# Kernel optimization log

Hardware: AMD Instinct MI355X
Metric: run time of the kernel (lower is better)

The kernel has to match this reference:

```python
import jax, jax.numpy as jnp
import numpy as np

B, S, H, M = 32, 512, 1024, 8  # batch, seq_len, HP_hidden_dim, term_span (max span length)


def setup_inputs() -> dict:
    key = jax.random.key(0)
    ks = jax.random.split(key, 6)
    return {
        "hidden_states": jax.random.normal(ks[0], (B, S, H), jnp.float32),
        "term_weight": jax.random.normal(ks[1], (H,), jnp.float32),          # nn.Parameter termWeight
        "w_in": jax.random.normal(ks[2], (H, H), jnp.float32) / np.float32(np.sqrt(H)),  # TermAttention.linear_in weight
        "b_in": jnp.zeros((H,), jnp.float32),                                 # TermAttention.linear_in bias
        "score_w": jax.random.normal(ks[3], (H,), jnp.float32) / np.float32(np.sqrt(H)),  # spanEmb2Score weight
        "score_b": jnp.zeros((), jnp.float32),                                # spanEmb2Score bias
        "seq_lengths": jnp.full((B,), S, jnp.int32),                          # full-length sentences (K is then static)
        "gold_mask": jax.random.randint(ks[4], (B, S, M), 0, 20, jnp.int32),
    }


def reference(hidden_states, term_weight, w_in, b_in, score_w, score_b, seq_lengths, gold_mask):
    B_, S_, H_ = hidden_states.shape
    M_ = gold_mask.shape[-1]

    # TermAttention: query = linear_in(termWeight)
    query = jnp.dot(w_in, term_weight) + b_in  # [H]

    pos = jnp.arange(S_)[:, None] + jnp.arange(M_)[None, :]          # [S, M]
    win = jnp.take(hidden_states, jnp.clip(pos, 0, S_ - 1), axis=1)  # [B, S, M, H]

    # Attention logits: dot(hidden, query), softmax over span positions per span length l+1
    logits = jnp.einsum('bsmh,h->bsm', win, query)                   # [B, S, M]
    m_idx = jnp.arange(M_)
    pos_mask = m_idx[None, :] < (m_idx[:, None] + 1)                 # [L, M]: position m valid for span length l+1
    masked = jnp.where(pos_mask[None, None], logits[:, :, None, :], -jnp.inf)  # [B, S, L, M]
    att = jax.nn.softmax(masked, axis=-1)
    pooled = jnp.einsum('bslm,bsmh->bslh', att, win)                 # [B, S, L, H] attention-pooled span reps

    # spanEmb2Score: Linear(H, 1)
    scores = jnp.einsum('bslh,h->bsl', pooled, score_w) + score_b    # [B, S, L]

    # Valid (deduplicated) spans: (s, s+l+1) kept iff s + l + 1 <= seq_len (matches set-dedup of clipped ends)
    span_valid = (jnp.arange(S_)[None, :, None] + m_idx[None, None, :] + 1) <= seq_lengths[:, None, None]
    gold = (gold_mask == 0) & span_valid

    # SoftMarginLoss: target 1 for gold spans, target 0 for all other spans -> constant log(2) term (faithful)
    per_span = jnp.where(gold, jax.nn.softplus(-scores), jnp.log(2.0).astype(scores.dtype))
    n_valid = jnp.sum(span_valid).astype(scores.dtype)
    loss = jnp.sum(jnp.where(span_valid, per_span, 0.0)) / n_valid

    # Precision@K, K = floor(0.3 * total_words); static since all sentences are full length
    K = int(0.3 * B_ * S_)
    flat_scores = jnp.where(span_valid, scores, -jnp.inf).reshape(-1)
    _, top_idx = jax.lax.top_k(flat_scores, K)
    right = jnp.sum(gold.reshape(-1)[top_idx])
    precision = right / K
    return loss, precision
```

## Files before the change

### kernel.cpp

```cpp
#include <hip/hip_runtime.h>

#define BB 32
#define SS 512
#define HH 1024
#define MM 8
#define NROWS (BB*SS)
#define NSPANS (BB*SS*MM)
#define KSEL 4915

constexpr size_t OFF_QUERY = 0;
constexpr size_t OFF_QD    = 4096;
constexpr size_t OFF_SD    = OFF_QD + 65536;
constexpr size_t OFF_KEYS  = OFF_SD + 65536;
constexpr size_t OFF_GOLD  = OFF_KEYS + 524288;
constexpr size_t OFF_H0    = OFF_GOLD + 524288;
constexpr size_t OFF_H1    = OFF_H0 + 1024;
constexpr size_t OFF_H2    = OFF_H1 + 1024;
constexpr size_t OFF_H3    = OFF_H2 + 1024;
constexpr size_t OFF_SCAL  = OFF_H3 + 1024;
constexpr size_t OFF_EQ    = OFF_SCAL + 64;
constexpr size_t ZERO_FROM  = OFF_H0;
constexpr size_t ZERO_BYTES = OFF_EQ - OFF_H0;

struct Scal {
    float    loss_sum;
    unsigned n_valid;
    unsigned p8,  R0;
    unsigned p16, R1;
    unsigned p24, R2;
    unsigned tau, T;
    unsigned right_gt, eq_count;
};

__device__ __forceinline__ unsigned sortable_key(float f) {
    unsigned b = __float_as_uint(f);
    return (b & 0x80000000u) ? ~b : (b | 0x80000000u);
}

__global__ void k_query(const float* __restrict__ w_in, const float* __restrict__ tw,
                        const float* __restrict__ b_in, float* __restrict__ query) {
    int wave = (blockIdx.x * blockDim.x + threadIdx.x) >> 6;
    int lane = threadIdx.x & 63;
    if (wave >= HH) return;
    const float4* wrow = (const float4*)(w_in + (size_t)wave * HH);
    const float4* tv   = (const float4*)tw;
    float s = 0.f;
    #pragma unroll
    for (int p = 0; p < 4; ++p) {
        int c = p * 64 + lane;
        float4 w = wrow[c]; float4 t = tv[c];
        s += w.x*t.x + w.y*t.y + w.z*t.z + w.w*t.w;
    }
    #pragma unroll
    for (int o = 32; o > 0; o >>= 1) s += __shfl_down(s, o);
    if (lane == 0) query[wave] = s + b_in[wave];
}

__global__ void k_dots(const float* __restrict__ hs, const float* __restrict__ query,
                       const float* __restrict__ sw, float* __restrict__ qd,
                       float* __restrict__ sd) {
    int wave = (blockIdx.x * blockDim.x + threadIdx.x) >> 6;
    int lane = threadIdx.x & 63;
    if (wave >= NROWS) return;
    const float4* row = (const float4*)(hs + (size_t)wave * HH);
    const float4* qv  = (const float4*)query;
    const float4* sv  = (const float4*)sw;
    float a = 0.f, c2 = 0.f;
    #pragma unroll
    for (int p = 0; p < 4; ++p) {
        int c = p * 64 + lane;
        float4 h = row[c]; float4 q = qv[c]; float4 w = sv[c];
        a  += h.x*q.x + h.y*q.y + h.z*q.z + h.w*q.w;
        c2 += h.x*w.x + h.y*w.y + h.z*w.z + h.w*w.w;
    }
    #pragma unroll
    for (int o = 32; o > 0; o >>= 1) { a += __shfl_down(a, o); c2 += __shfl_down(c2, o); }
    if (lane == 0) { qd[wave] = a; sd[wave] = c2; }
}

__global__ void k_scores(const float* __restrict__ qd, const float* __restrict__ sd,
                         const int* __restrict__ gold_mask, const int* __restrict__ seq_lengths,
                         const float* __restrict__ score_b_p,
                         unsigned* __restrict__ keys, unsigned* __restrict__ goldf,
                         unsigned* __restrict__ hist0, Scal* sc) {
    __shared__ unsigned h0[256];
    __shared__ float lsum[256];
    __shared__ int   lcnt[256];
    h0[threadIdx.x] = 0;
    __syncthreads();

    int t = blockIdx.x * blockDim.x + threadIdx.x;
    int b = t >> 9, s = t & (SS - 1);
    int seqlen = seq_lengths[b];
    float sb = *score_b_p;

    uint4 gm0 = ((const uint4*)gold_mask)[t * 2];
    uint4 gm1 = ((const uint4*)gold_mask)[t * 2 + 1];
    unsigned gmv[8] = {gm0.x, gm0.y, gm0.z, gm0.w, gm1.x, gm1.y, gm1.z, gm1.w};

    unsigned kbuf[8], gbuf[8];
    float lloss = 0.f; int lval = 0;
    float maxv = 0.f, den = 0.f, num = 0.f;
    #pragma unroll
    for (int m = 0; m < MM; ++m) {
        int pos = s + m; if (pos > SS - 1) pos = SS - 1;
        float x = qd[b * SS + pos];
        float v = sd[b * SS + pos];
        if (m == 0)         { maxv = x; den = 1.f; num = v; }
        else if (x > maxv)  { float e = expf(maxv - x); den = den * e + 1.f; num = num * e + v; maxv = x; }
        else                { float e = expf(x - maxv); den += e; num += e * v; }
        float score = num / den + sb;
        bool valid = (s + m + 1) <= seqlen;
        bool gold  = valid && (gmv[m] == 0u);
        unsigned key = valid ? sortable_key(score) : 0u;
        kbuf[m] = key;
        gbuf[m] = gold ? 1u : 0u;
        if (valid) {
            atomicAdd(&h0[key >> 24], 1u);
            lval++;
            float z = -score;
            float sp = (z > 0.f) ? (z + log1pf(expf(-z))) : log1pf(expf(z));
            lloss += gold ? sp : 0.69314718055994531f;
        }
    }
    ((uint4*)keys)[t * 2]     = make_uint4(kbuf[0], kbuf[1], kbuf[2], kbuf[3]);
    ((uint4*)keys)[t * 2 + 1] = make_uint4(kbuf[4], kbuf[5], kbuf[6], kbuf[7]);
    ((uint4*)goldf)[t * 2]     = make_uint4(gbuf[0], gbuf[1], gbuf[2], gbuf[3]);
    ((uint4*)goldf)[t * 2 + 1] = make_uint4(gbuf[4], gbuf[5], gbuf[6], gbuf[7]);

    lsum[threadIdx.x] = lloss; lcnt[threadIdx.x] = lval;
    __syncthreads();
    unsigned hv = h0[threadIdx.x];
    if (hv) atomicAdd(&hist0[threadIdx.x], hv);
    for (int o = 128; o > 0; o >>= 1) {
        if (threadIdx.x < o) { lsum[threadIdx.x] += lsum[threadIdx.x + o]; lcnt[threadIdx.x] += lcnt[threadIdx.x + o]; }
        __syncthreads();
    }
    if (threadIdx.x == 0) {
        atomicAdd(&sc->loss_sum, lsum[0]);
        atomicAdd(&sc->n_valid, (unsigned)lcnt[0]);
    }
}

__global__ void k_hist8(const unsigned* __restrict__ keys,
                        const unsigned* __restrict__ prev_hist,
                        unsigned* __restrict__ out_hist,
                        Scal* sc, int level) {
    __shared__ unsigned sh[256];
    __shared__ unsigned sres[2];
    sh[threadIdx.x] = prev_hist[threadIdx.x];
    __syncthreads();
    if (threadIdx.x == 0) {
        unsigned Rin, pprev;
        if (level == 1)      { Rin = KSEL;    pprev = 0; }
        else if (level == 2) { Rin = sc->R0;  pprev = sc->p8; }
        else                 { Rin = sc->R1;  pprev = sc->p16; }
        unsigned cum = 0; int c = 255;
        for (; c > 0; --c) { unsigned h = sh[c]; if (cum + h >= Rin) break; cum += h; }
        sres[0] = (pprev << 8) | (unsigned)c;
        sres[1] = Rin - cum;
    }
    __syncthreads();
    unsigned pref = sres[0], newR = sres[1];
    if (blockIdx.x == 0 && threadIdx.x == 0) {
        if (level == 1)      { sc->p8  = pref; sc->R0 = newR; }
        else if (level == 2) { sc->p16 = pref; sc->R1 = newR; }
        else                 { sc->p24 = pref; sc->R2 = newR; }
    }
    sh[threadIdx.x] = 0;
    __syncthreads();
    int shift  = (level == 1) ? 16 : (level == 2) ? 8 : 0;
    int mshift = shift + 8;
    for (int i = blockIdx.x * blockDim.x + threadIdx.x; i < NSPANS; i += gridDim.x * blockDim.x) {
        unsigned k = keys[i];
        if (k != 0u && (k >> mshift) == pref) atomicAdd(&sh[(k >> shift) & 0xFFu], 1u);
    }
    __syncthreads();
    unsigned v = sh[threadIdx.x];
    if (v) atomicAdd(&out_hist[threadIdx.x], v);
}

__global__ void k_count(const unsigned* __restrict__ keys, const unsigned* __restrict__ goldf,
                        const unsigned* __restrict__ hist3,
                        unsigned* __restrict__ eqList, Scal* sc) {
    __shared__ unsigned sh[256];
    __shared__ unsigned sres[2];
    sh[threadIdx.x] = hist3[threadIdx.x];
    __syncthreads();
    if (threadIdx.x == 0) {
        unsigned Rin = sc->R2, pprev = sc->p24;
        unsigned cum = 0; int c = 255;
        for (; c > 0; --c) { unsigned h = sh[c]; if (cum + h >= Rin) break; cum += h; }
        sres[0] = (pprev << 8) | (unsigned)c;
        sres[1] = Rin - cum;
    }
    __syncthreads();
    unsigned tau = sres[0], T = sres[1];
    if (blockIdx.x == 0 && threadIdx.x == 0) { sc->tau = tau; sc->T = T; }
    int lgt = 0;
    for (int i = blockIdx.x * blockDim.x + threadIdx.x; i < NSPANS; i += gridDim.x * blockDim.x) {
        unsigned k = keys[i];
        if (k > tau) lgt += (int)goldf[i];
        else if (k == tau) {
            unsigned p = atomicAdd(&sc->eq_count, 1u);
            if (p < 4096) eqList[p] = (unsigned)i;
        }
    }
    #pragma unroll
    for (int o = 32; o > 0; o >>= 1) lgt += __shfl_down(lgt, o);
    if ((threadIdx.x & 63) == 0 && lgt) atomicAdd(&sc->right_gt, (unsigned)lgt);
}

__global__ void k_final(const unsigned* __restrict__ goldf, const unsigned* __restrict__ eqList,
                        const Scal* sc, float* __restrict__ out) {
    if (blockIdx.x != 0 || threadIdx.x != 0) return;
    unsigned T = sc->T;
    unsigned neq = sc->eq_count; if (neq > 4096) neq = 4096;
    unsigned extra = 0;
    if (T >= neq) {
        for (unsigned i = 0; i < neq; ++i) extra += goldf[eqList[i]];
    } else {
        unsigned prev = 0; bool first = true;
        for (unsigned it = 0; it < T; ++it) {
            unsigned mn = 0xFFFFFFFFu;
            for (unsigned i = 0; i < neq; ++i) {
                unsigned v = eqList[i];
                if ((first || v > prev) && v < mn) mn = v;
            }
            if (mn == 0xFFFFFFFFu) break;
            extra += goldf[mn];
            prev = mn; first = false;
        }
    }
    float loss = sc->loss_sum / (float)sc->n_valid;
    float prec = (float)(sc->right_gt + extra) / (float)KSEL;
    out[0] = loss;
    out[1] = prec;
}

extern "C" void kernel_launch(void* const* d_in, const int* in_sizes, int n_in,
                              void* d_out, int out_size, void* d_ws, size_t ws_size,
                              hipStream_t stream) {
    const float* hidden   = (const float*)d_in[0];
    const float* term_w   = (const float*)d_in[1];
    const float* w_in     = (const float*)d_in[2];
    const float* b_in     = (const float*)d_in[3];
    const float* score_w  = (const float*)d_in[4];
    const float* score_b  = (const float*)d_in[5];
    const int*   seq_len  = (const int*)d_in[6];
    const int*   gmask    = (const int*)d_in[7];
    float* out            = (float*)d_out;

    char* ws = (char*)d_ws;
    float*    query = (float*)(ws + OFF_QUERY);
    float*    qd    = (float*)(ws + OFF_QD);
    float*    sd    = (float*)(ws + OFF_SD);
    unsigned* keys  = (unsigned*)(ws + OFF_KEYS);
    unsigned* goldf = (unsigned*)(ws + OFF_GOLD);
    unsigned* h0    = (unsigned*)(ws + OFF_H0);
    unsigned* h1    = (unsigned*)(ws + OFF_H1);
    unsigned* h2    = (unsigned*)(ws + OFF_H2);
    unsigned* h3    = (unsigned*)(ws + OFF_H3);
    unsigned* eqL   = (unsigned*)(ws + OFF_EQ);
    Scal*     sc    = (Scal*)(ws + OFF_SCAL);

    hipMemsetAsync(ws + ZERO_FROM, 0, ZERO_BYTES, stream);

    k_query <<<256, 256, 0, stream>>>(w_in, term_w, b_in, query);
    k_dots  <<<4096, 256, 0, stream>>>(hidden, query, score_w, qd, sd);
    k_scores<<<64, 256, 0, stream>>>(qd, sd, gmask, seq_len, score_b, keys, goldf, h0, sc);
    k_hist8 <<<128, 256, 0, stream>>>(keys, h0, h1, sc, 1);
    k_hist8 <<<128, 256, 0, stream>>>(keys, h1, h2, sc, 2);
    k_hist8 <<<128, 256, 0, stream>>>(keys, h2, h3, sc, 3);
    k_count <<<128, 256, 0, stream>>>(keys, goldf, h3, eqL, sc);
    k_final <<<1, 64, 0, stream>>>(goldf, eqL, sc, out);
}
```

Baseline: 151.2 us.

## Fuse score, radix-select and count stages into one cooperative kernel

Merges the scoring, three radix-histogram passes, counting and final kernels into one cooperative kernel of 64 blocks that uses grid-wide syncs between phases. The memset is folded into the query kernel, and the serial per-block bucket search becomes a parallel suffix scan. This removes several kernel launches and the memset, which matter because each post-processing stage is tiny. In exchange, each histogram pass now runs on only 64 blocks instead of 128, grid syncs add their own cost, and the cooperative launch has some overhead.

```diff
diff --git a/kernel.cpp b/kernel.cpp
--- a/kernel.cpp
+++ b/kernel.cpp
@@ -1,4 +1,7 @@
 #include <hip/hip_runtime.h>
+#include <hip/hip_cooperative_groups.h>
+
+namespace cg = cooperative_groups;
 
 #define BB 32
 #define SS 512
@@ -19,17 +22,14 @@
 constexpr size_t OFF_H3    = OFF_H2 + 1024;
 constexpr size_t OFF_SCAL  = OFF_H3 + 1024;
 constexpr size_t OFF_EQ    = OFF_SCAL + 64;
-constexpr size_t ZERO_FROM  = OFF_H0;
-constexpr size_t ZERO_BYTES = OFF_EQ - OFF_H0;
+constexpr unsigned ZERO_WORDS = (unsigned)((OFF_EQ - OFF_H0) / 4);
 
 struct Scal {
     float    loss_sum;
     unsigned n_valid;
-    unsigned p8,  R0;
-    unsigned p16, R1;
-    unsigned p24, R2;
+    unsigned right_gt;
+    unsigned eq_count;
     unsigned tau, T;
-    unsigned right_gt, eq_count;
 };
 
 __device__ __forceinline__ unsigned sortable_key(float f) {
@@ -38,7 +38,12 @@
 }
 
 __global__ void k_query(const float* __restrict__ w_in, const float* __restrict__ tw,
-                        const float* __restrict__ b_in, float* __restrict__ query) {
+                        const float* __restrict__ b_in, char* __restrict__ ws) {
+    if (blockIdx.x == 0) {
+        unsigned* z = (unsigned*)(ws + OFF_H0);
+        for (unsigned i = threadIdx.x; i < ZERO_WORDS; i += 256) z[i] = 0u;
+    }
+    float* query = (float*)(ws + OFF_QUERY);
     int wave = (blockIdx.x * blockDim.x + threadIdx.x) >> 6;
     int lane = threadIdx.x & 63;
     if (wave >= HH) return;
@@ -56,9 +61,11 @@
     if (lane == 0) query[wave] = s + b_in[wave];
 }
 
-__global__ void k_dots(const float* __restrict__ hs, const float* __restrict__ query,
-                       const float* __restrict__ sw, float* __restrict__ qd,
-                       float* __restrict__ sd) {
+__global__ void k_dots(const float* __restrict__ hs, const float* __restrict__ sw,
+                       char* __restrict__ ws) {
+    const float* query = (const float*)(ws + OFF_QUERY);
+    float* qd = (float*)(ws + OFF_QD);
+    float* sd = (float*)(ws + OFF_SD);
     int wave = (blockIdx.x * blockDim.x + threadIdx.x) >> 6;
     int lane = threadIdx.x & 63;
     if (wave >= NROWS) return;
@@ -78,164 +85,190 @@
     if (lane == 0) { qd[wave] = a; sd[wave] = c2; }
 }
 
-__global__ void k_scores(const float* __restrict__ qd, const float* __restrict__ sd,
-                         const int* __restrict__ gold_mask, const int* __restrict__ seq_lengths,
-                         const float* __restrict__ score_b_p,
-                         unsigned* __restrict__ keys, unsigned* __restrict__ goldf,
-                         unsigned* __restrict__ hist0, Scal* sc) {
-    __shared__ unsigned h0[256];
+__device__ __forceinline__ void block_sel(const unsigned* __restrict__ gh, unsigned Rin,
+                                          unsigned* sbuf, unsigned* sres, int tid,
+                                          unsigned& c, unsigned& rem) {
+    __syncthreads();
+    sbuf[tid] = gh[tid];
+    __syncthreads();
+    #pragma unroll
+    for (int off = 1; off < 256; off <<= 1) {
+        unsigned v = (tid + off < 256) ? sbuf[tid + off] : 0u;
+        __syncthreads();
+        sbuf[tid] += v;
+        __syncthreads();
+    }
+    unsigned Scur  = sbuf[tid];
+    unsigned Snext = (tid < 255) ? sbuf[tid + 1] : 0u;
+    if (Scur >= Rin && Snext < Rin) { sres[0] = (unsigned)tid; sres[1] = Rin - Snext; }
+    __syncthreads();
+    c = sres[0]; rem = sres[1];
+}
+
+__global__ __launch_bounds__(256)
+void k_post(char* __restrict__ ws, const int* __restrict__ gold_mask,
+            const int* __restrict__ seq_lengths, const float* __restrict__ score_b_p,
+            float* __restrict__ out) {
+    cg::grid_group grid = cg::this_grid();
+
+    const float* qd = (const float*)(ws + OFF_QD);
+    const float* sd = (const float*)(ws + OFF_SD);
+    unsigned* keys  = (unsigned*)(ws + OFF_KEYS);
+    unsigned* goldf = (unsigned*)(ws + OFF_GOLD);
+    unsigned* h0    = (unsigned*)(ws + OFF_H0);
+    unsigned* h1    = (unsigned*)(ws + OFF_H1);
+    unsigned* h2    = (unsigned*)(ws + OFF_H2);
+    unsigned* h3    = (unsigned*)(ws + OFF_H3);
+    unsigned* eqL   = (unsigned*)(ws + OFF_EQ);
+    Scal*     sc    = (Scal*)(ws + OFF_SCAL);
+
+    __shared__ unsigned hloc[256];
+    __shared__ unsigned sbuf[256];
+    __shared__ unsigned sres[2];
     __shared__ float lsum[256];
     __shared__ int   lcnt[256];
-    h0[threadIdx.x] = 0;
-    __syncthreads();
-
-    int t = blockIdx.x * blockDim.x + threadIdx.x;
-    int b = t >> 9, s = t & (SS - 1);
-    int seqlen = seq_lengths[b];
-    float sb = *score_b_p;
-
-    uint4 gm0 = ((const uint4*)gold_mask)[t * 2];
-    uint4 gm1 = ((const uint4*)gold_mask)[t * 2 + 1];
-    unsigned gmv[8] = {gm0.x, gm0.y, gm0.z, gm0.w, gm1.x, gm1.y, gm1.z, gm1.w};
-
-    unsigned kbuf[8], gbuf[8];
-    float lloss = 0.f; int lval = 0;
-    float maxv = 0.f, den = 0.f, num = 0.f;
-    #pragma unroll
-    for (int m = 0; m < MM; ++m) {
-        int pos = s + m; if (pos > SS - 1) pos = SS - 1;
-        float x = qd[b * SS + pos];
-        float v = sd[b * SS + pos];
-        if (m == 0)         { maxv = x; den = 1.f; num = v; }
-        else if (x > maxv)  { float e = expf(maxv - x); den = den * e + 1.f; num = num * e + v; maxv = x; }
-        else                { float e = expf(x - maxv); den += e; num += e * v; }
-        float score = num / den + sb;
-        bool valid = (s + m + 1) <= seqlen;
-        bool gold  = valid && (gmv[m] == 0u);
-        unsigned key = valid ? sortable_key(score) : 0u;
-        kbuf[m] = key;
-        gbuf[m] = gold ? 1u : 0u;
-        if (valid) {
-            atomicAdd(&h0[key >> 24], 1u);
-            lval++;
-            float z = -score;
-            float sp = (z > 0.f) ? (z + log1pf(expf(-z))) : log1pf(expf(z));
-            lloss += gold ? sp : 0.69314718055994531f;
-        }
-    }
-    ((uint4*)keys)[t * 2]     = make_uint4(kbuf[0], kbuf[1], kbuf[2], kbuf[3]);
-    ((uint4*)keys)[t * 2 + 1] = make_uint4(kbuf[4], kbuf[5], kbuf[6], kbuf[7]);
-    ((uint4*)goldf)[t * 2]     = make_uint4(gbuf[0], gbuf[1], gbuf[2], gbuf[3]);
-    ((uint4*)goldf)[t * 2 + 1] = make_uint4(gbuf[4], gbuf[5], gbuf[6], gbuf[7]);
-
-    lsum[threadIdx.x] = lloss; lcnt[threadIdx.x] = lval;
-    __syncthreads();
-    unsigned hv = h0[threadIdx.x];
-    if (hv) atomicAdd(&hist0[threadIdx.x], hv);
+
+    int tid = threadIdx.x;
+    int t   = blockIdx.x * 256 + tid;
+
+    hloc[tid] = 0;
+    __syncthreads();
+    {
+        int b = t >> 9, s = t & (SS - 1);
+        int seqlen = seq_lengths[b];
+        float sb = *score_b_p;
+
+        uint4 gm0 = ((const uint4*)gold_mask)[t * 2];
+        uint4 gm1 = ((const uint4*)gold_mask)[t * 2 + 1];
+        unsigned gmv[8] = {gm0.x, gm0.y, gm0.z, gm0.w, gm1.x, gm1.y, gm1.z, gm1.w};
+
+        unsigned kbuf[8], gbuf[8];
+        float lloss = 0.f; int lval = 0;
+        float maxv = 0.f, den = 0.f, num = 0.f;
+        #pragma unroll
+        for (int m = 0; m < MM; ++m) {
+            int pos = s + m; if (pos > SS - 1) pos = SS - 1;
+            float x = qd[b * SS + pos];
+            float v = sd[b * SS + pos];
+            if (m == 0)         { maxv = x; den = 1.f; num = v; }
+            else if (x > maxv)  { float e = expf(maxv - x); den = den * e + 1.f; num = num * e + v; maxv = x; }
+            else                { float e = expf(x - maxv); den += e; num += e * v; }
+            float score = num / den + sb;
+            bool valid = (s + m + 1) <= seqlen;
+            bool gold  = valid && (gmv[m] == 0u);
+            unsigned key = valid ? sortable_key(score) : 0u;
+            kbuf[m] = key;
+            gbuf[m] = gold ? 1u : 0u;
+            if (valid) {
+                atomicAdd(&hloc[key >> 24], 1u);
+                lval++;
+                float z = -score;
+                float sp = (z > 0.f) ? (z + log1pf(expf(-z))) : log1pf(expf(z));
+                lloss += gold ? sp : 0.69314718055994531f;
+            }
+        }
+        ((uint4*)keys)[t * 2]      = make_uint4(kbuf[0], kbuf[1], kbuf[2], kbuf[3]);
+        ((uint4*)keys)[t * 2 + 1]  = make_uint4(kbuf[4], kbuf[5], kbuf[6], kbuf[7]);
+        ((uint4*)goldf)[t * 2]     = make_uint4(gbuf[0], gbuf[1], gbuf[2], gbuf[3]);
+        ((uint4*)goldf)[t * 2 + 1] = make_uint4(gbuf[4], gbuf[5], gbuf[6], gbuf[7]);
+
+        lsum[tid] = lloss; lcnt[tid] = lval;
+    }
+    __syncthreads();
+    { unsigned hv = hloc[tid]; if (hv) atomicAdd(&h0[tid], hv); }
     for (int o = 128; o > 0; o >>= 1) {
-        if (threadIdx.x < o) { lsum[threadIdx.x] += lsum[threadIdx.x + o]; lcnt[threadIdx.x] += lcnt[threadIdx.x + o]; }
-        __syncthreads();
-    }
-    if (threadIdx.x == 0) {
+        if (tid < o) { lsum[tid] += lsum[tid + o]; lcnt[tid] += lcnt[tid + o]; }
+        __syncthreads();
+    }
+    if (tid == 0) {
         atomicAdd(&sc->loss_sum, lsum[0]);
         atomicAdd(&sc->n_valid, (unsigned)lcnt[0]);
     }
-}
-
-__global__ void k_hist8(const unsigned* __restrict__ keys,
-                        const unsigned* __restrict__ prev_hist,
-                        unsigned* __restrict__ out_hist,
-                        Scal* sc, int level) {
-    __shared__ unsigned sh[256];
-    __shared__ unsigned sres[2];
-    sh[threadIdx.x] = prev_hist[threadIdx.x];
-    __syncthreads();
-    if (threadIdx.x == 0) {
-        unsigned Rin, pprev;
-        if (level == 1)      { Rin = KSEL;    pprev = 0; }
-        else if (level == 2) { Rin = sc->R0;  pprev = sc->p8; }
-        else                 { Rin = sc->R1;  pprev = sc->p16; }
-        unsigned cum = 0; int c = 255;
-        for (; c > 0; --c) { unsigned h = sh[c]; if (cum + h >= Rin) break; cum += h; }
-        sres[0] = (pprev << 8) | (unsigned)c;
-        sres[1] = Rin - cum;
-    }
-    __syncthreads();
-    unsigned pref = sres[0], newR = sres[1];
-    if (blockIdx.x == 0 && threadIdx.x == 0) {
-        if (level == 1)      { sc->p8  = pref; sc->R0 = newR; }
-        else if (level == 2) { sc->p16 = pref; sc->R1 = newR; }
-        else                 { sc->p24 = pref; sc->R2 = newR; }
-    }
-    sh[threadIdx.x] = 0;
-    __syncthreads();
-    int shift  = (level == 1) ? 16 : (level == 2) ? 8 : 0;
-    int mshift = shift + 8;
-    for (int i = blockIdx.x * blockDim.x + threadIdx.x; i < NSPANS; i += gridDim.x * blockDim.x) {
+    grid.sync();
+
+    unsigned c0, r0, c1, r1, c2, r2, c3, r3;
+
+    block_sel(h0, KSEL, sbuf, sres, tid, c0, r0);
+    hloc[tid] = 0;
+    __syncthreads();
+    for (int i = t; i < NSPANS; i += NROWS) {
         unsigned k = keys[i];
-        if (k != 0u && (k >> mshift) == pref) atomicAdd(&sh[(k >> shift) & 0xFFu], 1u);
-    }
-    __syncthreads();
-    unsigned v = sh[threadIdx.x];
-    if (v) atomicAdd(&out_hist[threadIdx.x], v);
-}
-
-__global__ void k_count(const unsigned* __restrict__ keys, const unsigned* __restrict__ goldf,
-                        const unsigned* __restrict__ hist3,
-                        unsigned* __restrict__ eqList, Scal* sc) {
-    __shared__ unsigned sh[256];
-    __shared__ unsigned sres[2];
-    sh[threadIdx.x] = hist3[threadIdx.x];
-    __syncthreads();
-    if (threadIdx.x == 0) {
-        unsigned Rin = sc->R2, pprev = sc->p24;
-        unsigned cum = 0; int c = 255;
-        for (; c > 0; --c) { unsigned h = sh[c]; if (cum + h >= Rin) break; cum += h; }
-        sres[0] = (pprev << 8) | (unsigned)c;
-        sres[1] = Rin - cum;
-    }
-    __syncthreads();
-    unsigned tau = sres[0], T = sres[1];
-    if (blockIdx.x == 0 && threadIdx.x == 0) { sc->tau = tau; sc->T = T; }
-    int lgt = 0;
-    for (int i = blockIdx.x * blockDim.x + threadIdx.x; i < NSPANS; i += gridDim.x * blockDim.x) {
-        unsigned k = keys[i];
-        if (k > tau) lgt += (int)goldf[i];
-        else if (k == tau) {
-            unsigned p = atomicAdd(&sc->eq_count, 1u);
-            if (p < 4096) eqList[p] = (unsigned)i;
-        }
-    }
-    #pragma unroll
-    for (int o = 32; o > 0; o >>= 1) lgt += __shfl_down(lgt, o);
-    if ((threadIdx.x & 63) == 0 && lgt) atomicAdd(&sc->right_gt, (unsigned)lgt);
-}
-
-__global__ void k_final(const unsigned* __restrict__ goldf, const unsigned* __restrict__ eqList,
-                        const Scal* sc, float* __restrict__ out) {
-    if (blockIdx.x != 0 || threadIdx.x != 0) return;
-    unsigned T = sc->T;
-    unsigned neq = sc->eq_count; if (neq > 4096) neq = 4096;
-    unsigned extra = 0;
-    if (T >= neq) {
-        for (unsigned i = 0; i < neq; ++i) extra += goldf[eqList[i]];
-    } else {
-        unsigned prev = 0; bool first = true;
-        for (unsigned it = 0; it < T; ++it) {
-            unsigned mn = 0xFFFFFFFFu;
-            for (unsigned i = 0; i < neq; ++i) {
-                unsigned v = eqList[i];
-                if ((first || v > prev) && v < mn) mn = v;
+        if (k != 0u && (k >> 24) == c0) atomicAdd(&hloc[(k >> 16) & 0xFFu], 1u);
+    }
+    __syncthreads();
+    { unsigned v = hloc[tid]; if (v) atomicAdd(&h1[tid], v); }
+    grid.sync();
+
+    block_sel(h1, r0, sbuf, sres, tid, c1, r1);
+    {
+        unsigned pref = (c0 << 8) | c1;
+        hloc[tid] = 0;
+        __syncthreads();
+        for (int i = t; i < NSPANS; i += NROWS) {
+            unsigned k = keys[i];
+            if (k != 0u && (k >> 16) == pref) atomicAdd(&hloc[(k >> 8) & 0xFFu], 1u);
+        }
+        __syncthreads();
+        unsigned v = hloc[tid]; if (v) atomicAdd(&h2[tid], v);
+    }
+    grid.sync();
+
+    block_sel(h2, r1, sbuf, sres, tid, c2, r2);
+    {
+        unsigned pref = (c0 << 16) | (c1 << 8) | c2;
+        hloc[tid] = 0;
+        __syncthreads();
+        for (int i = t; i < NSPANS; i += NROWS) {
+            unsigned k = keys[i];
+            if (k != 0u && (k >> 8) == pref) atomicAdd(&hloc[k & 0xFFu], 1u);
+        }
+        __syncthreads();
+        unsigned v = hloc[tid]; if (v) atomicAdd(&h3[tid], v);
+    }
+    grid.sync();
+
+    block_sel(h3, r2, sbuf, sres, tid, c3, r3);
+    unsigned tau = (c0 << 24) | (c1 << 16) | (c2 << 8) | c3;
+    unsigned T   = r3;
+    {
+        int lgt = 0;
+        for (int i = t; i < NSPANS; i += NROWS) {
+            unsigned k = keys[i];
+            if (k > tau) lgt += (int)goldf[i];
+            else if (k == tau) {
+                unsigned p = atomicAdd(&sc->eq_count, 1u);
+                if (p < 4096) eqL[p] = (unsigned)i;
             }
-            if (mn == 0xFFFFFFFFu) break;
-            extra += goldf[mn];
-            prev = mn; first = false;
-        }
-    }
-    float loss = sc->loss_sum / (float)sc->n_valid;
-    float prec = (float)(sc->right_gt + extra) / (float)KSEL;
-    out[0] = loss;
-    out[1] = prec;
+        }
+        #pragma unroll
+        for (int o = 32; o > 0; o >>= 1) lgt += __shfl_down(lgt, o);
+        if ((tid & 63) == 0 && lgt) atomicAdd(&sc->right_gt, (unsigned)lgt);
+    }
+    grid.sync();
+
+    if (blockIdx.x == 0 && tid == 0) {
+        unsigned neq = sc->eq_count; if (neq > 4096) neq = 4096;
+        unsigned extra = 0;
+        if (T >= neq) {
+            for (unsigned i = 0; i < neq; ++i) extra += goldf[eqL[i]];
+        } else {
+            unsigned prev = 0; bool first = true;
+            for (unsigned it = 0; it < T; ++it) {
+                unsigned mn = 0xFFFFFFFFu;
+                for (unsigned i = 0; i < neq; ++i) {
+                    unsigned v = eqL[i];
+                    if ((first || v > prev) && v < mn) mn = v;
+                }
+                if (mn == 0xFFFFFFFFu) break;
+                extra += goldf[mn];
+                prev = mn; first = false;
+            }
+        }
+        float loss = sc->loss_sum / (float)sc->n_valid;
+        float prec = (float)(sc->right_gt + extra) / (float)KSEL;
+        out[0] = loss;
+        out[1] = prec;
+    }
 }
 
 extern "C" void kernel_launch(void* const* d_in, const int* in_sizes, int n_in,
@@ -250,28 +283,12 @@
     const int*   seq_len  = (const int*)d_in[6];
     const int*   gmask    = (const int*)d_in[7];
     float* out            = (float*)d_out;
-
-    char* ws = (char*)d_ws;
-    float*    query = (float*)(ws + OFF_QUERY);
-    float*    qd    = (float*)(ws + OFF_QD);
-    float*    sd    = (float*)(ws + OFF_SD);
-    unsigned* keys  = (unsigned*)(ws + OFF_KEYS);
-    unsigned* goldf = (unsigned*)(ws + OFF_GOLD);
-    unsigned* h0    = (unsigned*)(ws + OFF_H0);
-    unsigned* h1    = (unsigned*)(ws + OFF_H1);
-    unsigned* h2    = (unsigned*)(ws + OFF_H2);
-    unsigned* h3    = (unsigned*)(ws + OFF_H3);
-    unsigned* eqL   = (unsigned*)(ws + OFF_EQ);
-    Scal*     sc    = (Scal*)(ws + OFF_SCAL);
-
-    hipMemsetAsync(ws + ZERO_FROM, 0, ZERO_BYTES, stream);
-
-    k_query <<<256, 256, 0, stream>>>(w_in, term_w, b_in, query);
-    k_dots  <<<4096, 256, 0, stream>>>(hidden, query, score_w, qd, sd);
-    k_scores<<<64, 256, 0, stream>>>(qd, sd, gmask, seq_len, score_b, keys, goldf, h0, sc);
-    k_hist8 <<<128, 256, 0, stream>>>(keys, h0, h1, sc, 1);
-    k_hist8 <<<128, 256, 0, stream>>>(keys, h1, h2, sc, 2);
-    k_hist8 <<<128, 256, 0, stream>>>(keys, h2, h3, sc, 3);
-    k_count <<<128, 256, 0, stream>>>(keys, goldf, h3, eqL, sc);
-    k_final <<<1, 64, 0, stream>>>(goldf, eqL, sc, out);
-}
+    char*  ws             = (char*)d_ws;
+
+    k_query<<<256, 256, 0, stream>>>(w_in, term_w, b_in, ws);
+    k_dots <<<4096, 256, 0, stream>>>(hidden, score_w, ws);
+
+    void* args[] = { (void*)&ws, (void*)&gmask, (void*)&seq_len,
+                     (void*)&score_b, (void*)&out };
+    hipLaunchCooperativeKernel((void*)k_post, dim3(64), dim3(256), args, 0, stream);
+}
```

Result: slower. 193.9 us (+28.3%).
